# Kernel optimization log

Measured on AMD Instinct MI355X. Metric: run time of the kernel, lower is better.

## Reference

```python
import jax, jax.numpy as jnp
import numpy as np


def gcn_conv(x, W, b, src, dst, n_nodes):
    """PyG GCNConv: add self-loops, symmetric deg^-1/2 normalization,
    linear transform, scatter-add aggregation, bias."""
    loops = jnp.arange(n_nodes, dtype=src.dtype)
    s = jnp.concatenate([src, loops])  # sources (incl. self-loops)
    d = jnp.concatenate([dst, loops])  # targets
    deg = jax.ops.segment_sum(jnp.ones_like(d, dtype=x.dtype), d, num_segments=n_nodes)
    dinv = jnp.where(deg > 0, jax.lax.rsqrt(deg), 0.0)
    norm = dinv[s] * dinv[d]  # [E+N]
    h = x @ W  # [N, out]
    msg = h[s] * norm[:, None]  # [E+N, out]
    out = jax.ops.segment_sum(msg, d, num_segments=n_nodes)
    return out + b


def setup_inputs() -> dict:
    key = jax.random.key(0)
    ks = jax.random.split(key, 8)
    N, E, D, H = 50000, 600000, 128, 128
    x = jax.random.normal(ks[0], (N, D), dtype=jnp.float32)
    edge_index = jax.random.randint(ks[1], (2, E), 0, N, dtype=jnp.int64)
    sd = lambda fi: 1.0 / np.sqrt(fi)
    W1 = jax.random.normal(ks[2], (D, H), dtype=jnp.float32) * sd(D)
    b1 = jnp.zeros((H,), dtype=jnp.float32)
    W2 = jax.random.normal(ks[3], (H, H), dtype=jnp.float32) * sd(H)
    b2 = jnp.zeros((H,), dtype=jnp.float32)
    Wd = jax.random.normal(ks[4], (H, D), dtype=jnp.float32) * sd(H)
    bd = jnp.zeros((D,), dtype=jnp.float32)
    return {"x": x, "edge_index": edge_index, "W1": W1, "b1": b1,
            "W2": W2, "b2": b2, "Wd": Wd, "bd": bd}


def reference(x, edge_index, W1, b1, W2, b2, Wd, bd):
    n_nodes = x.shape[0]
    src, dst = edge_index[0], edge_index[1]
    h = gcn_conv(x, W1, b1, src, dst, n_nodes)
    h = jax.nn.relu(h)
    h = gcn_conv(h, W2, b2, src, dst, n_nodes)
    out = jax.nn.relu(h @ Wd + bd)  # decoder: Linear + ReLU
    return out
```

## Files before the change

kernel.cpp:

```cpp
#include <hip/hip_runtime.h>

typedef long long i64;
typedef __attribute__((ext_vector_type(8))) short short8;
typedef __attribute__((ext_vector_type(8))) unsigned short us8;
typedef __attribute__((ext_vector_type(4))) float f32x4;

#define DEG_STRIDE 64

__device__ __forceinline__ unsigned short bf16_rtn(float x) {
  unsigned u = __float_as_uint(x);
  unsigned r = (u + 0x7FFFu + ((u >> 16) & 1u)) >> 16;
  return (unsigned short)r;
}
__device__ __forceinline__ float bf16_to_f(unsigned short h) {
  return __uint_as_float(((unsigned)h) << 16);
}

__device__ __forceinline__ bool wave_is64(const int* __restrict__ ei32, i64 e0) {
  int probe = ei32[2 * e0 + 1];
  return __ballot(probe != 0) == 0ULL;
}

__global__ __launch_bounds__(256) void init_kernel(
    int* __restrict__ cnt, int N,
    const float* __restrict__ Wa, unsigned short* __restrict__ wha, unsigned short* __restrict__ wla,
    const float* __restrict__ Wb, unsigned short* __restrict__ whb, unsigned short* __restrict__ wlb,
    const float* __restrict__ Wc, unsigned short* __restrict__ whc, unsigned short* __restrict__ wlc) {
  int nbInit = (N + 255) >> 8;
  int bid = blockIdx.x;
  if (bid < nbInit) {
    int i = bid * 256 + threadIdx.x;
    if (i < N) cnt[i] = 0;
    return;
  }
  bid -= nbInit;
  int b = bid >> 6;
  int t = (bid & 63) * 256 + threadIdx.x;
  const float* W = (b == 0) ? Wa : (b == 1) ? Wb : Wc;
  unsigned short* wh = (b == 0) ? wha : (b == 1) ? whb : whc;
  unsigned short* wl = (b == 0) ? wla : (b == 1) ? wlb : wlc;
  int c = t >> 7, k = t & 127;
  float w = W[k * 128 + c];
  unsigned short hi = bf16_rtn(w);
  unsigned short lo = bf16_rtn(w - bf16_to_f(hi));
  wh[c * 128 + k] = hi;
  wl[c * 128 + k] = lo;
}

__global__ __launch_bounds__(256) void fill_kernel(const int* __restrict__ ei32,
                                                   int* __restrict__ cnt,
                                                   int* __restrict__ col, int E, int N) {
  int shard = blockIdx.x & 3;
  int chunk = blockIdx.x >> 2;
  int ns = (N + 3) >> 2;
  int lo = shard * ns, hi = min(lo + ns, N);
  int base = chunk * 2048;
  int t = threadIdx.x;
  bool is64 = wave_is64(ei32, min((i64)(base + t), (i64)E - 1));
#pragma unroll
  for (int j = 0; j < 8; ++j) {
    int e = base + j * 256 + t;
    if (e >= E) break;
    int d = is64 ? ei32[2 * ((i64)E + e)] : ei32[(i64)E + e];
    if (d >= lo && d < hi) {
      int s = is64 ? ei32[2 * (i64)e] : ei32[e];
      int pos = atomicAdd(&cnt[d], 1);
      if (pos < DEG_STRIDE) col[(i64)d * DEG_STRIDE + pos] = s;
    }
  }
}

template <int ABF16, int OUT>
__global__ __launch_bounds__(256, 2) void gemm_mfma(
    const void* __restrict__ Av, const unsigned short* __restrict__ WhT,
    const unsigned short* __restrict__ WlT, const float* __restrict__ bias,
    const int* __restrict__ cnt, void* __restrict__ outv, int N) {
  int tid = threadIdx.x;
  int wid = tid >> 6, lane = tid & 63;
  int lr = lane & 15, kg = (lane >> 4) * 8;
  int rowbase = blockIdx.x * 128 + wid * 32;

  f32x4 acc[2][8];
#pragma unroll
  for (int tr = 0; tr < 2; ++tr)
#pragma unroll
    for (int tc = 0; tc < 8; ++tc) acc[tr][tc] = (f32x4){0.f, 0.f, 0.f, 0.f};

  int r[2] = {rowbase + lr, rowbase + 16 + lr};

  for (int kc = 0; kc < 128; kc += 32) {
    int k0 = kc + kg;
    short8 afh[2], afl[2];
#pragma unroll
    for (int tr = 0; tr < 2; ++tr) {
      if (ABF16) {
        const unsigned short* Ab = (const unsigned short*)Av;
        us8 v = {0, 0, 0, 0, 0, 0, 0, 0};
        if (r[tr] < N) v = *reinterpret_cast<const us8*>(&Ab[(i64)r[tr] * 128 + k0]);
#pragma unroll
        for (int j = 0; j < 8; ++j) afh[tr][j] = (short)v[j];
      } else {
        const float* A = (const float*)Av;
        float4 va = make_float4(0.f, 0.f, 0.f, 0.f), vb = va;
        if (r[tr] < N) {
          const float* p = &A[(i64)r[tr] * 128 + k0];
          va = *reinterpret_cast<const float4*>(p);
          vb = *reinterpret_cast<const float4*>(p + 4);
        }
        float xs[8] = {va.x, va.y, va.z, va.w, vb.x, vb.y, vb.z, vb.w};
#pragma unroll
        for (int j = 0; j < 8; ++j) {
          unsigned short h = bf16_rtn(xs[j]);
          afh[tr][j] = (short)h;
          afl[tr][j] = (short)bf16_rtn(xs[j] - bf16_to_f(h));
        }
      }
    }
#pragma unroll
    for (int tc = 0; tc < 8; ++tc) {
      int c = tc * 16 + lr;
      short8 bfh = *reinterpret_cast<const short8*>(&WhT[c * 128 + k0]);
      short8 bfl = *reinterpret_cast<const short8*>(&WlT[c * 128 + k0]);
#pragma unroll
      for (int tr = 0; tr < 2; ++tr) {
        acc[tr][tc] = __builtin_amdgcn_mfma_f32_16x16x32_bf16(afh[tr], bfh, acc[tr][tc], 0, 0, 0);
        acc[tr][tc] = __builtin_amdgcn_mfma_f32_16x16x32_bf16(afh[tr], bfl, acc[tr][tc], 0, 0, 0);
        if (!ABF16)
          acc[tr][tc] = __builtin_amdgcn_mfma_f32_16x16x32_bf16(afl[tr], bfh, acc[tr][tc], 0, 0, 0);
      }
    }
  }

  if (OUT == 0) {
    unsigned short* hb = (unsigned short*)outv;
#pragma unroll
    for (int tr = 0; tr < 2; ++tr) {
#pragma unroll
      for (int reg = 0; reg < 4; ++reg) {
        int row = rowbase + tr * 16 + (lane >> 4) * 4 + reg;
        if (row >= N) continue;
        float dv = rsqrtf((float)cnt[row] + 1.0f);
#pragma unroll
        for (int tc = 0; tc < 8; ++tc) {
          int colg = tc * 16 + lr;
          hb[(i64)row * 128 + colg] = bf16_rtn(acc[tr][tc][reg] * dv);
        }
      }
    }
  } else {
    float* out = (float*)outv;
#pragma unroll
    for (int tr = 0; tr < 2; ++tr) {
#pragma unroll
      for (int reg = 0; reg < 4; ++reg) {
        int row = rowbase + tr * 16 + (lane >> 4) * 4 + reg;
        if (row >= N) continue;
#pragma unroll
        for (int tc = 0; tc < 8; ++tc) {
          int colg = tc * 16 + lr;
          float v = fmaxf(acc[tr][tc][reg] + bias[colg], 0.f);
          __builtin_nontemporal_store(v, &out[(i64)row * 128 + colg]);
        }
      }
    }
  }
}

template <int RELU>
__global__ __launch_bounds__(256) void agg_bf16(
    const unsigned short* __restrict__ hb, const int* __restrict__ col,
    const int* __restrict__ cnt, const float* __restrict__ bias,
    unsigned short* __restrict__ zout, int N) {
  int t = threadIdx.x;
  int lane = t & 63;
  int v = blockIdx.x * 16 + ((t >> 6) << 2) + (lane >> 4);
  int cl = lane & 15;
  if (v >= N) return;
  i64 base = (i64)v * 128 + cl * 8;
  us8 sv = *reinterpret_cast<const us8*>(&hb[base]);
  float a[8];
#pragma unroll
  for (int j = 0; j < 8; ++j) a[j] = bf16_to_f(sv[j]);

  int n = cnt[v];
  int end = min(n, DEG_STRIDE);
  const int* bucket = &col[(i64)v * DEG_STRIDE];
  int i = 0;
  for (; i + 7 < end; i += 8) {
    us8 u[8];
#pragma unroll
    for (int q = 0; q < 8; ++q)
      u[q] = *reinterpret_cast<const us8*>(&hb[(i64)bucket[i + q] * 128 + cl * 8]);
#pragma unroll
    for (int j = 0; j < 8; ++j)
      a[j] += ((bf16_to_f(u[0][j]) + bf16_to_f(u[1][j])) + (bf16_to_f(u[2][j]) + bf16_to_f(u[3][j]))) +
              ((bf16_to_f(u[4][j]) + bf16_to_f(u[5][j])) + (bf16_to_f(u[6][j]) + bf16_to_f(u[7][j])));
  }
  if (i + 3 < end) {
    us8 u[4];
#pragma unroll
    for (int q = 0; q < 4; ++q)
      u[q] = *reinterpret_cast<const us8*>(&hb[(i64)bucket[i + q] * 128 + cl * 8]);
#pragma unroll
    for (int j = 0; j < 8; ++j)
      a[j] += (bf16_to_f(u[0][j]) + bf16_to_f(u[1][j])) + (bf16_to_f(u[2][j]) + bf16_to_f(u[3][j]));
    i += 4;
  }
  for (; i < end; ++i) {
    us8 u0 = *reinterpret_cast<const us8*>(&hb[(i64)bucket[i] * 128 + cl * 8]);
#pragma unroll
    for (int j = 0; j < 8; ++j) a[j] += bf16_to_f(u0[j]);
  }

  float dv = rsqrtf((float)n + 1.0f);
  f32x4 b0 = *reinterpret_cast<const f32x4*>(&bias[cl * 8]);
  f32x4 b1 = *reinterpret_cast<const f32x4*>(&bias[cl * 8 + 4]);
  float rbias[8] = {b0[0], b0[1], b0[2], b0[3], b1[0], b1[1], b1[2], b1[3]};
  us8 o;
#pragma unroll
  for (int j = 0; j < 8; ++j) {
    float r = fmaf(a[j], dv, rbias[j]);
    if (RELU) r = fmaxf(r, 0.f);
    o[j] = bf16_rtn(r);
  }
  __builtin_nontemporal_store(o, reinterpret_cast<us8*>(&zout[base]));
}

extern "C" void kernel_launch(void* const* d_in, const int* in_sizes, int n_in,
                              void* d_out, int out_size, void* d_ws, size_t ws_size,
                              hipStream_t stream) {
  const float* x  = (const float*)d_in[0];
  const int*   ei = (const int*)d_in[1];
  const float* W1 = (const float*)d_in[2];
  const float* b1 = (const float*)d_in[3];
  const float* W2 = (const float*)d_in[4];
  const float* b2 = (const float*)d_in[5];
  const float* Wd = (const float*)d_in[6];
  const float* bd = (const float*)d_in[7];
  int N = in_sizes[0] / 128;
  int E = in_sizes[1] / 2;
  float* out = (float*)d_out;

  char* w = (char*)d_ws;
  unsigned short* zb   = (unsigned short*)w;
  unsigned short* wh1  = zb + (i64)N * 128;
  unsigned short* wl1  = wh1 + 16384;
  unsigned short* wh2  = wl1 + 16384;
  unsigned short* wl2  = wh2 + 16384;
  unsigned short* whd  = wl2 + 16384;
  unsigned short* wld  = whd + 16384;
  int*   cnt    = (int*)(wld + 16384);
  int*   col    = cnt + N;
  unsigned short* hb = (unsigned short*)d_out;

  int nbInit = (N + 255) / 256;
  int cb = (E + 2047) / 2048;
  int gblocks = (N + 127) / 128;
  int ablocks = (N + 15) / 16;

  init_kernel<<<nbInit + 192, 256, 0, stream>>>(cnt, N,
      W1, wh1, wl1, W2, wh2, wl2, Wd, whd, wld);
  fill_kernel<<<4 * cb, 256, 0, stream>>>(ei, cnt, col, E, N);

  gemm_mfma<0, 0><<<gblocks, 256, 0, stream>>>(x, wh1, wl1, nullptr, cnt, hb, N);
  agg_bf16<1><<<ablocks, 256, 0, stream>>>(hb, col, cnt, b1, zb, N);
  gemm_mfma<1, 0><<<gblocks, 256, 0, stream>>>(zb, wh2, wl2, nullptr, cnt, hb, N);
  agg_bf16<0><<<ablocks, 256, 0, stream>>>(hb, col, cnt, b2, zb, N);
  gemm_mfma<1, 1><<<gblocks, 256, 0, stream>>>(zb, whd, wld, bd, cnt, out, N);
}
```

Before: 165.4 us.

## Store hidden features in column-chunked slabs to localize aggregation gathers

The GEMM now writes its bf16 output as eight column slabs of 16 features each (slab-major layout) instead of row-major rows of 128. The aggregation kernel assigns each block to one slab, so its neighbour gathers touch a compact 1.6MB array that can stay in cache, at the cost of 8-byte gathers per lane instead of 16-byte. Each slab is read by separate blocks, so neighbour indices are read eight times and each gather moves less data per request.

```diff
diff --git a/kernel.cpp b/kernel.cpp
--- a/kernel.cpp
+++ b/kernel.cpp
@@ -3,6 +3,7 @@
 typedef long long i64;
 typedef __attribute__((ext_vector_type(8))) short short8;
 typedef __attribute__((ext_vector_type(8))) unsigned short us8;
+typedef __attribute__((ext_vector_type(4))) unsigned short us4;
 typedef __attribute__((ext_vector_type(4))) float f32x4;
 
 #define DEG_STRIDE 64
@@ -142,8 +143,7 @@
         float dv = rsqrtf((float)cnt[row] + 1.0f);
 #pragma unroll
         for (int tc = 0; tc < 8; ++tc) {
-          int colg = tc * 16 + lr;
-          hb[(i64)row * 128 + colg] = bf16_rtn(acc[tr][tc][reg] * dv);
+          hb[(i64)tc * N * 16 + (i64)row * 16 + lr] = bf16_rtn(acc[tr][tc][reg] * dv);
         }
       }
     }
@@ -171,59 +171,67 @@
     const unsigned short* __restrict__ hb, const int* __restrict__ col,
     const int* __restrict__ cnt, const float* __restrict__ bias,
     unsigned short* __restrict__ zout, int N) {
+  int chunk = blockIdx.x & 7;
+  int nbidx = blockIdx.x >> 3;
   int t = threadIdx.x;
-  int lane = t & 63;
-  int v = blockIdx.x * 16 + ((t >> 6) << 2) + (lane >> 4);
-  int cl = lane & 15;
+  int v = nbidx * 64 + (t >> 2);
+  int l4 = t & 3;
   if (v >= N) return;
-  i64 base = (i64)v * 128 + cl * 8;
-  us8 sv = *reinterpret_cast<const us8*>(&hb[base]);
-  float a[8];
-#pragma unroll
-  for (int j = 0; j < 8; ++j) a[j] = bf16_to_f(sv[j]);
+  const unsigned short* slab = hb + (i64)chunk * N * 16;
+
+  us4 sv = *reinterpret_cast<const us4*>(&slab[(i64)v * 16 + l4 * 4]);
+  float a0 = bf16_to_f(sv[0]), a1 = bf16_to_f(sv[1]);
+  float a2 = bf16_to_f(sv[2]), a3 = bf16_to_f(sv[3]);
 
   int n = cnt[v];
   int end = min(n, DEG_STRIDE);
   const int* bucket = &col[(i64)v * DEG_STRIDE];
   int i = 0;
   for (; i + 7 < end; i += 8) {
-    us8 u[8];
+    us4 u[8];
 #pragma unroll
     for (int q = 0; q < 8; ++q)
-      u[q] = *reinterpret_cast<const us8*>(&hb[(i64)bucket[i + q] * 128 + cl * 8]);
-#pragma unroll
-    for (int j = 0; j < 8; ++j)
-      a[j] += ((bf16_to_f(u[0][j]) + bf16_to_f(u[1][j])) + (bf16_to_f(u[2][j]) + bf16_to_f(u[3][j]))) +
-              ((bf16_to_f(u[4][j]) + bf16_to_f(u[5][j])) + (bf16_to_f(u[6][j]) + bf16_to_f(u[7][j])));
+      u[q] = *reinterpret_cast<const us4*>(&slab[(i64)bucket[i + q] * 16 + l4 * 4]);
+    a0 += ((bf16_to_f(u[0][0]) + bf16_to_f(u[1][0])) + (bf16_to_f(u[2][0]) + bf16_to_f(u[3][0]))) +
+          ((bf16_to_f(u[4][0]) + bf16_to_f(u[5][0])) + (bf16_to_f(u[6][0]) + bf16_to_f(u[7][0])));
+    a1 += ((bf16_to_f(u[0][1]) + bf16_to_f(u[1][1])) + (bf16_to_f(u[2][1]) + bf16_to_f(u[3][1]))) +
+          ((bf16_to_f(u[4][1]) + bf16_to_f(u[5][1])) + (bf16_to_f(u[6][1]) + bf16_to_f(u[7][1])));
+    a2 += ((bf16_to_f(u[0][2]) + bf16_to_f(u[1][2])) + (bf16_to_f(u[2][2]) + bf16_to_f(u[3][2]))) +
+          ((bf16_to_f(u[4][2]) + bf16_to_f(u[5][2])) + (bf16_to_f(u[6][2]) + bf16_to_f(u[7][2])));
+    a3 += ((bf16_to_f(u[0][3]) + bf16_to_f(u[1][3])) + (bf16_to_f(u[2][3]) + bf16_to_f(u[3][3]))) +
+          ((bf16_to_f(u[4][3]) + bf16_to_f(u[5][3])) + (bf16_to_f(u[6][3]) + bf16_to_f(u[7][3])));
   }
   if (i + 3 < end) {
-    us8 u[4];
+    us4 u[4];
 #pragma unroll
     for (int q = 0; q < 4; ++q)
-      u[q] = *reinterpret_cast<const us8*>(&hb[(i64)bucket[i + q] * 128 + cl * 8]);
-#pragma unroll
-    for (int j = 0; j < 8; ++j)
-      a[j] += (bf16_to_f(u[0][j]) + bf16_to_f(u[1][j])) + (bf16_to_f(u[2][j]) + bf16_to_f(u[3][j]));
+      u[q] = *reinterpret_cast<const us4*>(&slab[(i64)bucket[i + q] * 16 + l4 * 4]);
+    a0 += (bf16_to_f(u[0][0]) + bf16_to_f(u[1][0])) + (bf16_to_f(u[2][0]) + bf16_to_f(u[3][0]));
+    a1 += (bf16_to_f(u[0][1]) + bf16_to_f(u[1][1])) + (bf16_to_f(u[2][1]) + bf16_to_f(u[3][1]));
+    a2 += (bf16_to_f(u[0][2]) + bf16_to_f(u[1][2])) + (bf16_to_f(u[2][2]) + bf16_to_f(u[3][2]));
+    a3 += (bf16_to_f(u[0][3]) + bf16_to_f(u[1][3])) + (bf16_to_f(u[2][3]) + bf16_to_f(u[3][3]));
     i += 4;
   }
   for (; i < end; ++i) {
-    us8 u0 = *reinterpret_cast<const us8*>(&hb[(i64)bucket[i] * 128 + cl * 8]);
-#pragma unroll
-    for (int j = 0; j < 8; ++j) a[j] += bf16_to_f(u0[j]);
+    us4 u0 = *reinterpret_cast<const us4*>(&slab[(i64)bucket[i] * 16 + l4 * 4]);
+    a0 += bf16_to_f(u0[0]); a1 += bf16_to_f(u0[1]);
+    a2 += bf16_to_f(u0[2]); a3 += bf16_to_f(u0[3]);
   }
 
   float dv = rsqrtf((float)n + 1.0f);
-  f32x4 b0 = *reinterpret_cast<const f32x4*>(&bias[cl * 8]);
-  f32x4 b1 = *reinterpret_cast<const f32x4*>(&bias[cl * 8 + 4]);
-  float rbias[8] = {b0[0], b0[1], b0[2], b0[3], b1[0], b1[1], b1[2], b1[3]};
-  us8 o;
-#pragma unroll
-  for (int j = 0; j < 8; ++j) {
-    float r = fmaf(a[j], dv, rbias[j]);
-    if (RELU) r = fmaxf(r, 0.f);
-    o[j] = bf16_rtn(r);
-  }
-  __builtin_nontemporal_store(o, reinterpret_cast<us8*>(&zout[base]));
+  f32x4 b = *reinterpret_cast<const f32x4*>(&bias[chunk * 16 + l4 * 4]);
+  us4 o;
+  float r0 = fmaf(a0, dv, b[0]);
+  float r1 = fmaf(a1, dv, b[1]);
+  float r2 = fmaf(a2, dv, b[2]);
+  float r3 = fmaf(a3, dv, b[3]);
+  if (RELU) {
+    r0 = fmaxf(r0, 0.f); r1 = fmaxf(r1, 0.f);
+    r2 = fmaxf(r2, 0.f); r3 = fmaxf(r3, 0.f);
+  }
+  o[0] = bf16_rtn(r0); o[1] = bf16_rtn(r1);
+  o[2] = bf16_rtn(r2); o[3] = bf16_rtn(r3);
+  __builtin_nontemporal_store(o, reinterpret_cast<us4*>(&zout[(i64)v * 128 + chunk * 16 + l4 * 4]));
 }
 
 extern "C" void kernel_launch(void* const* d_in, const int* in_sizes, int n_in,
@@ -256,7 +264,7 @@
   int nbInit = (N + 255) / 256;
   int cb = (E + 2047) / 2048;
   int gblocks = (N + 127) / 128;
-  int ablocks = (N + 15) / 16;
+  int ablocks = 8 * ((N + 63) / 64);
 
   init_kernel<<<nbInit + 192, 256, 0, stream>>>(cnt, N,
       W1, wh1, wl1, W2, wh2, wl2, Wd, whd, wld);
```

Result: slower. 186.3 us (+12.6%).

## Store transformed features in column-chunked slabs for cache-local aggregation

Applied to the files above, without the earlier changes.

The first-stage GEMM now writes bf16 features as four column slabs of 32 features each, every slab laid out as N rows of 64 bytes. The aggregation kernel gives each block one slab and one half of the nodes, using 4 threads per node. The block index interleaves the 8 slab/half combinations so blocks running at the same time gather from a small working set of about 3.2 MB per slab, which is meant to raise L2 hit rates on the random neighbour gathers. The trade-off is 64-byte gather granularity in place of 256-byte rows, and the adjacency list and counts are now read once per slab instead of once per node.

```diff
diff --git a/kernel.cpp b/kernel.cpp
--- a/kernel.cpp
+++ b/kernel.cpp
@@ -142,8 +142,9 @@
         float dv = rsqrtf((float)cnt[row] + 1.0f);
 #pragma unroll
         for (int tc = 0; tc < 8; ++tc) {
-          int colg = tc * 16 + lr;
-          hb[(i64)row * 128 + colg] = bf16_rtn(acc[tr][tc][reg] * dv);
+          int chunk = tc >> 1;
+          int inner = ((tc & 1) << 4) + lr;
+          hb[(i64)chunk * N * 32 + (i64)row * 32 + inner] = bf16_rtn(acc[tr][tc][reg] * dv);
         }
       }
     }
@@ -170,14 +171,19 @@
 __global__ __launch_bounds__(256) void agg_bf16(
     const unsigned short* __restrict__ hb, const int* __restrict__ col,
     const int* __restrict__ cnt, const float* __restrict__ bias,
-    unsigned short* __restrict__ zout, int N) {
+    unsigned short* __restrict__ zout, int N, int halfN, int nbpp) {
+  int g = blockIdx.x & 7;
+  int chunk = g & 3;
+  int h = g >> 2;
+  int nb = blockIdx.x >> 3;
   int t = threadIdx.x;
-  int lane = t & 63;
-  int v = blockIdx.x * 16 + ((t >> 6) << 2) + (lane >> 4);
-  int cl = lane & 15;
-  if (v >= N) return;
-  i64 base = (i64)v * 128 + cl * 8;
-  us8 sv = *reinterpret_cast<const us8*>(&hb[base]);
+  int v = h * halfN + nb * 64 + (t >> 2);
+  int lim = h ? N : halfN;
+  if (v >= lim) return;
+  int cl = t & 3;
+  const unsigned short* slab = hb + (i64)chunk * N * 32;
+
+  us8 sv = *reinterpret_cast<const us8*>(&slab[(i64)v * 32 + cl * 8]);
   float a[8];
 #pragma unroll
   for (int j = 0; j < 8; ++j) a[j] = bf16_to_f(sv[j]);
@@ -190,7 +196,7 @@
     us8 u[8];
 #pragma unroll
     for (int q = 0; q < 8; ++q)
-      u[q] = *reinterpret_cast<const us8*>(&hb[(i64)bucket[i + q] * 128 + cl * 8]);
+      u[q] = *reinterpret_cast<const us8*>(&slab[(i64)bucket[i + q] * 32 + cl * 8]);
 #pragma unroll
     for (int j = 0; j < 8; ++j)
       a[j] += ((bf16_to_f(u[0][j]) + bf16_to_f(u[1][j])) + (bf16_to_f(u[2][j]) + bf16_to_f(u[3][j]))) +
@@ -200,21 +206,21 @@
     us8 u[4];
 #pragma unroll
     for (int q = 0; q < 4; ++q)
-      u[q] = *reinterpret_cast<const us8*>(&hb[(i64)bucket[i + q] * 128 + cl * 8]);
+      u[q] = *reinterpret_cast<const us8*>(&slab[(i64)bucket[i + q] * 32 + cl * 8]);
 #pragma unroll
     for (int j = 0; j < 8; ++j)
       a[j] += (bf16_to_f(u[0][j]) + bf16_to_f(u[1][j])) + (bf16_to_f(u[2][j]) + bf16_to_f(u[3][j]));
     i += 4;
   }
   for (; i < end; ++i) {
-    us8 u0 = *reinterpret_cast<const us8*>(&hb[(i64)bucket[i] * 128 + cl * 8]);
+    us8 u0 = *reinterpret_cast<const us8*>(&slab[(i64)bucket[i] * 32 + cl * 8]);
 #pragma unroll
     for (int j = 0; j < 8; ++j) a[j] += bf16_to_f(u0[j]);
   }
 
   float dv = rsqrtf((float)n + 1.0f);
-  f32x4 b0 = *reinterpret_cast<const f32x4*>(&bias[cl * 8]);
-  f32x4 b1 = *reinterpret_cast<const f32x4*>(&bias[cl * 8 + 4]);
+  f32x4 b0 = *reinterpret_cast<const f32x4*>(&bias[chunk * 32 + cl * 8]);
+  f32x4 b1 = *reinterpret_cast<const f32x4*>(&bias[chunk * 32 + cl * 8 + 4]);
   float rbias[8] = {b0[0], b0[1], b0[2], b0[3], b1[0], b1[1], b1[2], b1[3]};
   us8 o;
 #pragma unroll
@@ -223,7 +229,7 @@
     if (RELU) r = fmaxf(r, 0.f);
     o[j] = bf16_rtn(r);
   }
-  __builtin_nontemporal_store(o, reinterpret_cast<us8*>(&zout[base]));
+  __builtin_nontemporal_store(o, reinterpret_cast<us8*>(&zout[(i64)v * 128 + chunk * 32 + cl * 8]));
 }
 
 extern "C" void kernel_launch(void* const* d_in, const int* in_sizes, int n_in,
@@ -256,15 +262,17 @@
   int nbInit = (N + 255) / 256;
   int cb = (E + 2047) / 2048;
   int gblocks = (N + 127) / 128;
-  int ablocks = (N + 15) / 16;
+  int halfN = (N + 1) / 2;
+  int nbpp = (halfN + 63) / 64;
+  int ablocks = 8 * nbpp;
 
   init_kernel<<<nbInit + 192, 256, 0, stream>>>(cnt, N,
       W1, wh1, wl1, W2, wh2, wl2, Wd, whd, wld);
   fill_kernel<<<4 * cb, 256, 0, stream>>>(ei, cnt, col, E, N);
 
   gemm_mfma<0, 0><<<gblocks, 256, 0, stream>>>(x, wh1, wl1, nullptr, cnt, hb, N);
-  agg_bf16<1><<<ablocks, 256, 0, stream>>>(hb, col, cnt, b1, zb, N);
+  agg_bf16<1><<<ablocks, 256, 0, stream>>>(hb, col, cnt, b1, zb, N, halfN, nbpp);
   gemm_mfma<1, 0><<<gblocks, 256, 0, stream>>>(zb, wh2, wl2, nullptr, cnt, hb, N);
-  agg_bf16<0><<<ablocks, 256, 0, stream>>>(hb, col, cnt, b2, zb, N);
+  agg_bf16<0><<<ablocks, 256, 0, stream>>>(hb, col, cnt, b2, zb, N, halfN, nbpp);
   gemm_mfma<1, 1><<<gblocks, 256, 0, stream>>>(zb, whd, wld, bd, cnt, out, N);
 }
```

After: 166.0 us. Within noise of the previous version (+0.3%).
